# Kernel tuning notes

Measured on AMD Instinct MI355X. Metric: run time of the kernel, lower is better.

## Reference

```python
import jax, jax.numpy as jnp
import numpy as np

B, H, W, C = 8, 128, 128, 192
WS, SS, HEADS = 8, 4, 6
NW = (H // WS) * (W // WS)
N = WS * WS

def _rel_pos_index(ws):
    coords = np.stack(np.meshgrid(np.arange(ws), np.arange(ws), indexing='ij')).reshape(2, -1)
    rel = (coords[:, :, None] - coords[:, None, :]).transpose(1, 2, 0)
    rel[:, :, 0] += ws - 1
    rel[:, :, 1] += ws - 1
    rel[:, :, 0] *= 2 * ws - 1
    return rel.sum(-1)  # (N, N) int

REL_IDX = jnp.asarray(_rel_pos_index(WS).reshape(-1))

def setup_inputs():
    key = jax.random.key(0)
    ks = jax.random.split(key, 8)
    p = lambda k, shp: jax.random.normal(k, shp, jnp.float32) * 0.02
    # exact Swin shift mask for shift=(SS,SS)
    img = np.zeros((1, H, W, 1), np.float32)
    cnt = 0
    for hs in (slice(0, -WS), slice(-WS, -SS), slice(-SS, None)):
        for vs in (slice(0, -WS), slice(-WS, -SS), slice(-SS, None)):
            img[:, hs, vs, :] = cnt; cnt += 1
    mw = img.reshape(1, H // WS, WS, W // WS, WS, 1).transpose(0, 1, 3, 2, 4, 5).reshape(-1, N)
    diff = mw[:, None, :] - mw[:, :, None]
    mask = np.where(diff != 0, -100.0, 0.0).astype(np.float32)
    return dict(
        x=jax.random.normal(ks[0], (B, H, W, C), jnp.float32),
        mask_matrix=jnp.asarray(mask),
        norm1_g=jnp.ones((C,), jnp.float32), norm1_b=jnp.zeros((C,), jnp.float32),
        qkv_w=p(ks[1], (C, 3 * C)), qkv_b=jnp.zeros((3 * C,), jnp.float32),
        rel_bias_table=p(ks[2], ((2 * WS - 1) * (2 * WS - 1), HEADS)),
        proj_w=p(ks[3], (C, C)), proj_b=jnp.zeros((C,), jnp.float32),
        norm2_g=jnp.ones((C,), jnp.float32), norm2_b=jnp.zeros((C,), jnp.float32),
        fc1_w=p(ks[4], (C, 4 * C)), fc1_b=jnp.zeros((4 * C,), jnp.float32),
        fc2_w=p(ks[5], (4 * C, C)), fc2_b=jnp.zeros((C,), jnp.float32),
    )

def _ln(x, g, b):
    m = x.mean(-1, keepdims=True)
    v = x.var(-1, keepdims=True)
    return (x - m) * jax.lax.rsqrt(v + 1e-5) * g + b

def _window_attn(xw, mask, qkv_w, qkv_b, rel_bias_table, proj_w, proj_b):
    Bw = xw.shape[0]
    hd = C // HEADS
    scale = hd ** -0.5
    # ---- spatial window attention ----
    qkv = (xw @ qkv_w + qkv_b).reshape(Bw, N, 3, HEADS, hd).transpose(2, 0, 3, 1, 4)
    q, k, v = qkv[0], qkv[1], qkv[2]  # (Bw, heads, N, hd)
    attn = jnp.einsum('bhnd,bhmd->bhnm', q, k) * scale
    bias = rel_bias_table[REL_IDX].reshape(N, N, HEADS).transpose(2, 0, 1)
    attn = attn + bias[None]
    attn = attn.reshape(Bw // NW, NW, HEADS, N, N) + mask[None, :, None]
    attn = jax.nn.softmax(attn.reshape(Bw, HEADS, N, N), axis=-1)
    x_spatial = jnp.einsum('bhnm,bhmd->bhnd', attn, v).transpose(0, 2, 1, 3).reshape(Bw, N, C)
    # ---- Fourier-domain attention branch ----
    x2d = xw.reshape(Bw, WS, WS, C)
    xf = jnp.fft.rfftn(x2d, axes=(1, 2), norm='ortho')  # (Bw, WS, WS//2+1, C) complex
    Hf, Wf = xf.shape[1], xf.shape[2]
    Nf = Hf * Wf
    def _qkv(r):  # shared qkv linear applied to real/imag parts (bias in both)
        return (r.reshape(Bw, Nf, C) @ qkv_w + qkv_b).reshape(Bw, Nf, 3, HEADS, hd).transpose(2, 0, 3, 1, 4)
    qr, qi = _qkv(xf.real), _qkv(xf.imag)
    qf = jax.lax.complex(qr[0], qi[0])
    kf = jax.lax.complex(qr[1], qi[1])
    vf = jax.lax.complex(qr[2], qi[2])
    attn_f = jnp.einsum('bhnd,bhmd->bhnm', qf, kf) * scale  # plain transpose, no conj (matches torch)
    attn_mag = jax.nn.softmax(jnp.abs(attn_f), axis=-1)
    xf_res = jnp.einsum('bhnm,bhmd->bhnd', attn_mag.astype(jnp.complex64), vf)
    xf_res = xf_res.transpose(0, 2, 1, 3).reshape(Bw, Hf, Wf, C)
    x_four = jnp.fft.irfftn(xf_res, s=(WS, WS), axes=(1, 2), norm='ortho').reshape(Bw, N, C)
    return (x_spatial + x_four) @ proj_w + proj_b

def reference(x, mask_matrix, norm1_g, norm1_b, qkv_w, qkv_b, rel_bias_table,
              proj_w, proj_b, norm2_g, norm2_b, fc1_w, fc1_b, fc2_w, fc2_b):
    shortcut = x
    xn = _ln(x, norm1_g, norm1_b)
    # shift (H,W divisible by WS so no padding needed)
    xs = jnp.roll(xn, (-SS, -SS), axis=(1, 2))
    # window partition -> (B*nW, N, C)
    xw = xs.reshape(B, H // WS, WS, W // WS, WS, C).transpose(0, 1, 3, 2, 4, 5).reshape(-1, N, C)
    aw = _window_attn(xw, mask_matrix, qkv_w, qkv_b, rel_bias_table, proj_w, proj_b)
    # window reverse + unshift
    xs = aw.reshape(B, H // WS, W // WS, WS, WS, C).transpose(0, 1, 3, 2, 4, 5).reshape(B, H, W, C)
    xo = jnp.roll(xs, (SS, SS), axis=(1, 2))
    x1 = shortcut + xo
    y = _ln(x1, norm2_g, norm2_b)
    y = jax.nn.gelu(y @ fc1_w + fc1_b, approximate=False) @ fc2_w + fc2_b
    return x1 + y
```

## Files before the change

kernel.cpp:

```cpp
#include <hip/hip_runtime.h>
#include <hip/hip_bf16.h>
#include <math.h>

#define SSH 4
#define SCALE 0.17677669529663687f

typedef __bf16 bf16x8 __attribute__((ext_vector_type(8)));
typedef __bf16 bf16x4 __attribute__((ext_vector_type(4)));
typedef unsigned short ushort8 __attribute__((ext_vector_type(8)));
typedef float  f32x4  __attribute__((ext_vector_type(4)));

static __device__ __forceinline__ f32x4 mfma16(bf16x8 a, bf16x8 b, f32x4 c){
    return __builtin_amdgcn_mfma_f32_16x16x32_bf16(a, b, c, 0, 0, 0);
}
#define MFMA16(a,b,c) mfma16((a),(b),(c))

static __device__ __forceinline__ bf16x8 ldfrag(const __bf16* p){
    return *reinterpret_cast<const bf16x8*>(p);
}
static __device__ __forceinline__ f32x4 zero4(){
    f32x4 z; z[0]=0.f; z[1]=0.f; z[2]=0.f; z[3]=0.f; return z;
}
static __device__ __forceinline__ float gelu_fast(float x){
    float u = x*(0.7978845608f + 0.0356774081f*x*x);
    return __fdividef(x, 1.f + __expf(-2.f*u));
}

__global__ __launch_bounds__(256) void k_prep(const float* __restrict__ qkvw,
        const float* __restrict__ projw, const float* __restrict__ fc1w,
        const float* __restrict__ fc2w, __bf16* __restrict__ Wq,
        __bf16* __restrict__ Wp, __bf16* __restrict__ W1, __bf16* __restrict__ W2,
        __bf16* __restrict__ Fre, __bf16* __restrict__ Fim,
        __bf16* __restrict__ Ci,  __bf16* __restrict__ nSi){
    int i = blockIdx.x*256 + threadIdx.x;
    if (i < 110592){ int n = i/192, k = i - n*192; Wq[i] = (__bf16)qkvw[k*576 + n]; }
    if (i < 36864) { int n = i/192, k = i - n*192; Wp[i] = (__bf16)projw[k*192 + n]; }
    if (i < 147456){ int n = i/192, k = i - n*192; W1[i] = (__bf16)fc1w[k*768 + n]; }
    if (i < 147456){ int n = i/768, k = i - n*768; W2[i] = (__bf16)fc2w[k*192 + n]; }
    if (i < 3072){
        int n = i>>6, p = i&63;
        float vr = 0.f, vi = 0.f;
        if (n < 40){
            int u = n/5, v = n - u*5, r = p>>3, c = p&7;
            int k = (u*r + v*c)&7;
            float ang = (float)k * 0.78539816339744831f;
            vr = cosf(ang)*0.125f; vi = -sinf(ang)*0.125f;
        }
        Fre[i] = (__bf16)vr; Fim[i] = (__bf16)vi;
    }
    if (i < 4096){
        int p = i>>6, n = i&63;
        float vc = 0.f, vs = 0.f;
        if (n < 40){
            int u = n/5, v = n - u*5, r = p>>3, c = p&7;
            int k = (u*r + v*c)&7;
            float ang = (float)k * 0.78539816339744831f;
            float wv = (v>=1 && v<=3)? 2.f : 1.f;
            vc = wv*cosf(ang)*0.125f; vs = -wv*sinf(ang)*0.125f;
        }
        Ci[i] = (__bf16)vc; nSi[i] = (__bf16)vs;
    }
}

__global__ __launch_bounds__(256,2) void k_qkv(const float* __restrict__ x,
        const float* __restrict__ n1g, const float* __restrict__ n1b,
        const __bf16* __restrict__ Wqt, const float* __restrict__ qkv_b,
        __bf16* __restrict__ S){
    __shared__ __align__(16) __bf16 xw[64*200];
    __shared__ __align__(16) __bf16 Wt[192*72];
    __shared__ __align__(16) __bf16 Ss[64*200];
    int tid = threadIdx.x;
    int win = blockIdx.x;
    int bb = win>>8, rem = win&255, wh = rem>>4, wwi = rem&15;
    {
        int tok = tid>>2, part = tid&3;
        int r = tok>>3, c = tok&7;
        int sh = (wh*8 + r + SSH)&127, sw = (wwi*8 + c + SSH)&127;
        const float* srcp = x + (((size_t)(bb*128+sh))*128 + sw)*192 + part*48;
        float v[48];
        #pragma unroll
        for (int i=0;i<12;i++){
            float4 t4 = *reinterpret_cast<const float4*>(srcp + i*4);
            v[i*4]=t4.x; v[i*4+1]=t4.y; v[i*4+2]=t4.z; v[i*4+3]=t4.w;
        }
        float s=0.f, ss=0.f;
        #pragma unroll
        for (int i=0;i<48;i++){ s+=v[i]; ss+=v[i]*v[i]; }
        s  += __shfl_xor(s,1);  s  += __shfl_xor(s,2);
        ss += __shfl_xor(ss,1); ss += __shfl_xor(ss,2);
        float mean = s*(1.f/192.f);
        float rstd = rsqrtf(ss*(1.f/192.f) - mean*mean + 1e-5f);
        #pragma unroll
        for (int i8=0;i8<6;i8++){
            bf16x8 pk;
            #pragma unroll
            for (int j=0;j<8;j++){
                int ch = part*48 + i8*8 + j;
                pk[j] = (__bf16)((v[i8*8+j]-mean)*rstd*n1g[ch] + n1b[ch]);
            }
            *reinterpret_cast<bf16x8*>(&xw[tok*200 + part*48 + i8*8]) = pk;
        }
    }
    int lane = tid&63, w = tid>>6, lr = lane&15, lg = lane>>4;
    ushort8 wreg[6];
    auto ldW = [&](int s, ushort8* wr){
        int nc = s/3, kc = s - nc*3;
        #pragma unroll
        for (int i=0;i<6;i++){
            int e = tid + i*256;
            int j = e>>3, k8 = e&7;
            wr[i] = *reinterpret_cast<const ushort8*>(
                reinterpret_cast<const unsigned short*>(Wqt) + (size_t)(nc*192+j)*192 + kc*64 + k8*8);
        }
    };
    auto stW = [&](ushort8* wr){
        #pragma unroll
        for (int i=0;i<6;i++){
            int e = tid + i*256;
            int j = e>>3, k8 = e&7;
            *reinterpret_cast<ushort8*>(reinterpret_cast<unsigned short*>(Wt) + j*72 + k8*8) = wr[i];
        }
    };
    ldW(0, wreg);
    __syncthreads();
    stW(wreg);
    __syncthreads();
    f32x4 acc[4][3];
    #pragma unroll
    for (int m=0;m<4;m++)
        #pragma unroll
        for (int n=0;n<3;n++) acc[m][n] = zero4();
    for (int s=0; s<9; s++){
        int nc = s/3, kc = s - nc*3;
        if (s<8) ldW(s+1, wreg);
        #pragma unroll
        for (int kk=0; kk<2; kk++){
            int ko = kc*64 + kk*32 + lg*8;
            bf16x8 a[4];
            #pragma unroll
            for (int m=0;m<4;m++) a[m] = ldfrag(&xw[(16*m+lr)*200 + ko]);
            int klo = kk*32 + lg*8;
            bf16x8 bfr[3];
            #pragma unroll
            for (int n=0;n<3;n++) bfr[n] = ldfrag(&Wt[(48*w+16*n+lr)*72 + klo]);
            #pragma unroll
            for (int m=0;m<4;m++)
                #pragma unroll
                for (int n=0;n<3;n++) acc[m][n] = MFMA16(a[m], bfr[n], acc[m][n]);
        }
        if (kc==2){
            #pragma unroll
            for (int n=0;n<3;n++){
                int colL = 48*w + 16*n + lr;
                float bias = qkv_b[nc*192 + colL];
                #pragma unroll
                for (int m=0;m<4;m++)
                    #pragma unroll
                    for (int r=0;r<4;r++){
                        Ss[(16*m + 4*lg + r)*200 + colL] = (__bf16)(acc[m][n][r] + bias);
                        acc[m][n][r] = 0.f;
                    }
            }
        }
        __syncthreads();
        if (kc==2){
            #pragma unroll
            for (int i=0;i<6;i++){
                int e = tid + i*256;
                int row = e/24, c8 = e - row*24;
                *reinterpret_cast<bf16x8*>(S + (size_t)(win*64+row)*576 + nc*192 + c8*8) =
                    *reinterpret_cast<const bf16x8*>(&Ss[row*200 + c8*8]);
            }
        }
        if (s<8) stW(wreg);
        __syncthreads();
    }
}

__global__ __launch_bounds__(256,4) void k_spatial(const __bf16* __restrict__ S,
        const float* __restrict__ relt, const float* __restrict__ mask,
        float* __restrict__ Bbuf){
    __shared__ __align__(16) __bf16 P[64*72];
    __shared__ __align__(16) __bf16 Vt[32*72];
    __shared__ float reltL[1350];
    int tid = threadIdx.x;
    int win = blockIdx.x;
    int widx = win & 255;
    int lane = tid&63, w = tid>>6, lr = lane&15, lg = lane>>4;
    for (int e=tid; e<1350; e+=256) reltL[e] = relt[e];
    float mreg[16];
    int bidx[16];
    #pragma unroll
    for (int nt=0; nt<4; nt++)
        #pragma unroll
        for (int r=0;r<4;r++){
            int row = 16*w + 4*lg + r;
            int col = 16*nt + lr;
            mreg[nt*4+r] = mask[((widx*64 + row)<<6) + col];
            int dr = (row>>3)-(col>>3)+7, dc = (row&7)-(col&7)+7;
            bidx[nt*4+r] = (dr*15+dc)*6;
        }
    const size_t sbase = (size_t)win*64*576;
    const __bf16* Sq = S + sbase;
    const __bf16* Sk = S + sbase + 192;
    const __bf16* Sv = S + sbase + 384;
    for (int h=0; h<6; h++){
        __syncthreads();
        {
            int d = tid&31, pg = tid>>5;
            const __bf16* sp = Sv + (size_t)(pg*8)*576 + h*32 + d;
            bf16x4 v0, v1;
            v0[0]=sp[0];    v0[1]=sp[576];  v0[2]=sp[1152]; v0[3]=sp[1728];
            v1[0]=sp[2304]; v1[1]=sp[2880]; v1[2]=sp[3456]; v1[3]=sp[4032];
            *reinterpret_cast<bf16x4*>(&Vt[d*72 + pg*8])   = v0;
            *reinterpret_cast<bf16x4*>(&Vt[d*72 + pg*8+4]) = v1;
        }
        __syncthreads();
        bf16x8 aq = ldfrag(Sq + (size_t)(16*w+lr)*576 + h*32 + lg*8);
        f32x4 acc[4];
        #pragma unroll
        for (int nt=0;nt<4;nt++){
            bf16x8 bk = ldfrag(Sk + (size_t)(16*nt+lr)*576 + h*32 + lg*8);
            acc[nt] = MFMA16(aq, bk, zero4());
        }
        float p[16];
        #pragma unroll
        for (int r=0;r<4;r++){
            float sc[4];
            #pragma unroll
            for (int nt=0;nt<4;nt++)
                sc[nt] = acc[nt][r]*SCALE + reltL[bidx[nt*4+r] + h] + mreg[nt*4+r];
            float mx = fmaxf(fmaxf(sc[0],sc[1]),fmaxf(sc[2],sc[3]));
            mx = fmaxf(mx, __shfl_xor(mx,1));
            mx = fmaxf(mx, __shfl_xor(mx,2));
            mx = fmaxf(mx, __shfl_xor(mx,4));
            mx = fmaxf(mx, __shfl_xor(mx,8));
            float sum = 0.f;
            #pragma unroll
            for (int nt=0;nt<4;nt++){ sc[nt] = __expf(sc[nt]-mx); sum += sc[nt]; }
            sum += __shfl_xor(sum,1);
            sum += __shfl_xor(sum,2);
            sum += __shfl_xor(sum,4);
            sum += __shfl_xor(sum,8);
            float inv = 1.f/sum;
            #pragma unroll
            for (int nt=0;nt<4;nt++) p[r*4+nt] = sc[nt]*inv;
        }
        #pragma unroll
        for (int r=0;r<4;r++)
            #pragma unroll
            for (int nt=0;nt<4;nt++)
                P[(16*w + 4*lg + r)*72 + 16*nt + lr] = (__bf16)p[r*4+nt];
        #pragma unroll
        for (int dt=0; dt<2; dt++){
            f32x4 o = zero4();
            #pragma unroll
            for (int ks=0; ks<2; ks++)
                o = MFMA16(ldfrag(&P[(16*w+lr)*72 + ks*32 + lg*8]),
                           ldfrag(&Vt[(16*dt+lr)*72 + ks*32 + lg*8]), o);
            #pragma unroll
            for (int r=0;r<4;r++){
                int row = 16*w + 4*lg + r;
                Bbuf[((size_t)win*64 + row)*192 + h*32 + 16*dt + lr] = o[r];
            }
        }
    }
}

__global__ __launch_bounds__(256,3) void k_fattn(const __bf16* __restrict__ S,
        const float* __restrict__ qkv_b,
        const __bf16* __restrict__ Fre_g, const __bf16* __restrict__ Fim_g,
        const __bf16* __restrict__ Ci_g,  const __bf16* __restrict__ nSi_g,
        float* __restrict__ Bbuf){
    __shared__ __align__(16) unsigned char arena[51968];
    __bf16* Gq_r = (__bf16*)(arena);
    __bf16* Gqin = (__bf16*)(arena + 3840);
    __bf16* Gk_r = (__bf16*)(arena + 7680);
    __bf16* Gk_i = (__bf16*)(arena + 11520);
    __bf16* Rt_r = (__bf16*)(arena);
    __bf16* Rt_i = (__bf16*)(arena + 5632);
    __bf16* Gv_r = (__bf16*)(arena + 15360);
    __bf16* Gv_i = (__bf16*)(arena + 20992);
    __bf16* St3  = (__bf16*)(arena + 26624);
    float*  Smat = (float*) (arena + 26624);
    __bf16* P    = (__bf16*)(arena + 43520);
    int tid = threadIdx.x;
    int win = blockIdx.x / 6, h = blockIdx.x - win*6;
    int lane = tid&63, w = tid>>6, lr = lane&15, lg = lane>>4;
    bf16x4 z4; z4[0]=z4[1]=z4[2]=z4[3]=(__bf16)0.f;
    const size_t sbase = (size_t)win*64*576 + h*32;
    {
        int t2 = tid & 127;
        __bf16* A = (tid<128)? Gv_r : Gv_i;
        int row = t2>>2, c4 = (t2&3)*4;
        *reinterpret_cast<bf16x4*>(A + row*88 + 48 + c4) = z4;
    }
    {
        int d = tid&31, pg = tid>>5;
        #pragma unroll
        for (int m=0;m<3;m++){
            const __bf16* sp = S + sbase + (size_t)m*192 + (size_t)pg*8*576 + d;
            bf16x4 v0, v1;
            v0[0]=sp[0];      v0[1]=sp[576];    v0[2]=sp[1152];   v0[3]=sp[1728];
            v1[0]=sp[2304];   v1[1]=sp[2880];   v1[2]=sp[3456];   v1[3]=sp[4032];
            *reinterpret_cast<bf16x4*>(&St3[m*2816 + d*88 + pg*8])     = v0;
            *reinterpret_cast<bf16x4*>(&St3[m*2816 + d*88 + pg*8 + 4]) = v1;
        }
    }
    __syncthreads();
    for (int j=w; j<36; j+=4){
        int m = j/12, jj = j - m*12;
        int term = jj/6, r2 = jj - term*6;
        const __bf16* Stm = &St3[m*2816];
        if (m<2){
            int mt = r2>>1, nt = r2&1;
            const __bf16* Ag = (term? Fim_g : Fre_g) + (16*mt+lr)*64 + lg*8;
            f32x4 acc = zero4();
            acc = MFMA16(*reinterpret_cast<const bf16x8*>(Ag),
                         ldfrag(&Stm[(16*nt+lr)*88 + lg*8]), acc);
            acc = MFMA16(*reinterpret_cast<const bf16x8*>(Ag+32),
                         ldfrag(&Stm[(16*nt+lr)*88 + 32 + lg*8]), acc);
            int d = 16*nt + lr;
            float b = qkv_b[m*192 + h*32 + d];
            __bf16* dst = (m==0)? (term? Gqin : Gq_r) : (term? Gk_i : Gk_r);
            #pragma unroll
            for (int r=0;r<4;r++){
                int n = 16*mt + 4*lg + r;
                float val = acc[r] + ((term==0) ? ((n==0)? -7.f*b : b) : b);
                if (m==0 && term==1) val = -val;
                dst[n*40 + d] = (__bf16)val;
            }
        } else {
            int mt = r2/3, nt = r2 - mt*3;
            const __bf16* Bg = (term? Fim_g : Fre_g) + (16*nt+lr)*64 + lg*8;
            f32x4 acc = zero4();
            acc = MFMA16(ldfrag(&Stm[(16*mt+lr)*88 + lg*8]),
                         *reinterpret_cast<const bf16x8*>(Bg), acc);
            acc = MFMA16(ldfrag(&Stm[(16*mt+lr)*88 + 32 + lg*8]),
                         *reinterpret_cast<const bf16x8*>(Bg+32), acc);
            int n = 16*nt + lr;
            __bf16* dst = term? Gv_i : Gv_r;
            #pragma unroll
            for (int r=0;r<4;r++){
                int d = 16*mt + 4*lg + r;
                float b = qkv_b[2*192 + h*32 + d];
                float val = acc[r] + ((term==0) ? ((n==0)? -7.f*b : b) : b);
                dst[d*88 + n] = (__bf16)val;
            }
        }
    }
    __syncthreads();
    for (int j=w; j<9; j+=4){
        int mt = j/3, nt = j - mt*3;
        bf16x8 qr = ldfrag(&Gq_r[(16*mt+lr)*40 + lg*8]);
        bf16x8 qi = ldfrag(&Gqin[(16*mt+lr)*40 + lg*8]);
        bf16x8 kr = ldfrag(&Gk_r[(16*nt+lr)*40 + lg*8]);
        bf16x8 ki = ldfrag(&Gk_i[(16*nt+lr)*40 + lg*8]);
        f32x4 sre = MFMA16(qi, ki, zero4());
        sre = MFMA16(qr, kr, sre);
        f32x4 t1 = MFMA16(qr, ki, zero4());
        f32x4 t2 = MFMA16(qi, kr, zero4());
        #pragma unroll
        for (int r=0;r<4;r++){
            float sim = t1[r] - t2[r];
            Smat[(16*mt + 4*lg + r)*52 + 16*nt + lr] =
                SCALE * sqrtf(sre[r]*sre[r] + sim*sim);
        }
    }
    __syncthreads();
    if (tid < 160){
        int row = tid>>2, part = tid&3, e0 = part*10;
        float mx = -1e30f;
        #pragma unroll
        for (int j=0;j<10;j++) mx = fmaxf(mx, Smat[row*52 + e0 + j]);
        mx = fmaxf(mx, __shfl_xor(mx,1));
        mx = fmaxf(mx, __shfl_xor(mx,2));
        float ex[10]; float sum=0.f;
        #pragma unroll
        for (int j=0;j<10;j++){ ex[j] = __expf(Smat[row*52+e0+j]-mx); sum += ex[j]; }
        sum += __shfl_xor(sum,1);
        sum += __shfl_xor(sum,2);
        float inv = 1.f/sum;
        #pragma unroll
        for (int j=0;j<10;j++) Smat[row*52+e0+j] = ex[j]*inv;
    }
    __syncthreads();
    for (int e=tid; e<3072; e+=256){
        int row = e>>6, col = e&63;
        float v = (row<40 && col<40)? Smat[row*52+col] : 0.f;
        P[row*88+col] = (__bf16)v;
    }
    {
        int t2 = tid & 127;
        __bf16* A = (tid<128)? Rt_r : Rt_i;
        int row = t2>>2, c4 = (t2&3)*4;
        *reinterpret_cast<bf16x4*>(A + row*88 + 48 + c4) = z4;
    }
    __syncthreads();
    for (int j=w; j<12; j+=4){
        int term = j/6, r2 = j - term*6;
        int dt = r2/3, nt = r2 - dt*3;
        const __bf16* Gv = term? Gv_i : Gv_r;
        f32x4 acc = zero4();
        #pragma unroll
        for (int ks=0; ks<2; ks++)
            acc = MFMA16(ldfrag(&Gv[(16*dt+lr)*88 + ks*32 + lg*8]),
                         ldfrag(&P [(16*nt+lr)*88 + ks*32 + lg*8]), acc);
        __bf16* dst = term? Rt_i : Rt_r;
        #pragma unroll
        for (int r=0;r<4;r++)
            dst[(16*dt + 4*lg + r)*88 + 16*nt + lr] = (__bf16)acc[r];
    }
    __syncthreads();
    for (int j=w; j<8; j+=4){
        int dt = j>>2, pt = j&3;
        f32x4 acc = zero4();
        #pragma unroll
        for (int ks=0; ks<2; ks++)
            acc = MFMA16(*reinterpret_cast<const bf16x8*>(nSi_g + (16*pt+lr)*64 + ks*32 + lg*8),
                         ldfrag(&Rt_i[(16*dt+lr)*88 + ks*32 + lg*8]), acc);
        #pragma unroll
        for (int ks=0; ks<2; ks++)
            acc = MFMA16(*reinterpret_cast<const bf16x8*>(Ci_g + (16*pt+lr)*64 + ks*32 + lg*8),
                         ldfrag(&Rt_r[(16*dt+lr)*88 + ks*32 + lg*8]), acc);
        #pragma unroll
        for (int r=0;r<4;r++){
            int p = 16*pt + 4*lg + r, d = 16*dt + lr;
            size_t idx = ((size_t)win*64 + p)*192 + h*32 + d;
            Bbuf[idx] += acc[r];
        }
    }
}

__global__ __launch_bounds__(256,2) void k_ffn(const float* __restrict__ Bbuf,
        const float* __restrict__ x, const __bf16* __restrict__ Wpt,
        const float* __restrict__ proj_b, const float* __restrict__ g2,
        const float* __restrict__ b2v, const __bf16* __restrict__ W1t,
        const float* __restrict__ fc1b, const __bf16* __restrict__ W2t,
        const float* __restrict__ fc2b, float* __restrict__ out){
    __shared__ __align__(16) __bf16 xt[64*200];
    __shared__ __align__(16) __bf16 yb[64*200];
    int tid = threadIdx.x;
    int win = blockIdx.x;
    {
        int tok = tid>>2, part = tid&3;
        const float* srcp = Bbuf + ((size_t)win*64 + tok)*192 + part*48;
        #pragma unroll
        for (int i8=0;i8<6;i8++){
            float4 a4 = *reinterpret_cast<const float4*>(srcp + i8*8);
            float4 b4 = *reinterpret_cast<const float4*>(srcp + i8*8 + 4);
            bf16x8 pk;
            pk[0]=(__bf16)a4.x; pk[1]=(__bf16)a4.y; pk[2]=(__bf16)a4.z; pk[3]=(__bf16)a4.w;
            pk[4]=(__bf16)b4.x; pk[5]=(__bf16)b4.y; pk[6]=(__bf16)b4.z; pk[7]=(__bf16)b4.w;
            *reinterpret_cast<bf16x8*>(&xt[tok*200 + part*48 + i8*8]) = pk;
        }
    }
    __syncthreads();
    int lane = tid&63, w = tid>>6, lr = lane&15, lg = lane>>4;
    f32x4 acc[4][3];
    #pragma unroll
    for (int m=0;m<4;m++)
        #pragma unroll
        for (int n=0;n<3;n++) acc[m][n] = zero4();
    #pragma unroll
    for (int kc=0; kc<6; kc++){
        int ko = kc*32 + lg*8;
        bf16x8 a[4];
        #pragma unroll
        for (int m=0;m<4;m++) a[m] = ldfrag(&xt[(16*m+lr)*200 + ko]);
        bf16x8 bfr[3];
        #pragma unroll
        for (int n=0;n<3;n++)
            bfr[n] = ldfrag(Wpt + (size_t)(48*w + 16*n + lr)*192 + ko);
        #pragma unroll
        for (int m=0;m<4;m++)
            #pragma unroll
            for (int n=0;n<3;n++) acc[m][n] = MFMA16(a[m], bfr[n], acc[m][n]);
    }
    int bb = win>>8, rem = win&255, wh = rem>>4, wwi = rem&15;
    bf16x4 yreg[4][3];
    #pragma unroll
    for (int m=0;m<4;m++)
        #pragma unroll
        for (int r=0;r<4;r++){
            int t = 16*m + 4*lg + r;
            int p = wh*8 + (t>>3), q = wwi*8 + (t&7);
            int hh = (p+SSH)&127, w2 = (q+SSH)&127;
            size_t pixb = (((size_t)bb*128 + hh)*128 + w2)*192;
            #pragma unroll
            for (int n=0;n<3;n++){
                int col = 48*w + 16*n + lr;
                float yv = acc[m][n][r] + proj_b[col] + x[pixb + col];
                __bf16 yh = (__bf16)yv;
                yreg[m][n][r] = yh;
                yb[t*200 + col] = yh;
            }
        }
    __syncthreads();
    {
        int tok = tid>>2, part = tid&3;
        float v[48];
        #pragma unroll
        for (int i8=0;i8<6;i8++){
            bf16x8 pk = *reinterpret_cast<const bf16x8*>(&yb[tok*200 + part*48 + i8*8]);
            #pragma unroll
            for (int j=0;j<8;j++) v[i8*8+j] = (float)pk[j];
        }
        float s=0.f, ss=0.f;
        #pragma unroll
        for (int i=0;i<48;i++){ s+=v[i]; ss+=v[i]*v[i]; }
        s  += __shfl_xor(s,1);  s  += __shfl_xor(s,2);
        ss += __shfl_xor(ss,1); ss += __shfl_xor(ss,2);
        float mean = s*(1.f/192.f);
        float rstd = rsqrtf(ss*(1.f/192.f) - mean*mean + 1e-5f);
        #pragma unroll
        for (int i8=0;i8<6;i8++){
            bf16x8 pk;
            #pragma unroll
            for (int j=0;j<8;j++){
                int ch = part*48 + i8*8 + j;
                pk[j] = (__bf16)((v[i8*8+j]-mean)*rstd*g2[ch] + b2v[ch]);
            }
            *reinterpret_cast<bf16x8*>(&yb[tok*200 + part*48 + i8*8]) = pk;
        }
    }
    __syncthreads();
    f32x4 acc2[4][3];
    #pragma unroll
    for (int m=0;m<4;m++)
        #pragma unroll
        for (int n=0;n<3;n++) acc2[m][n] = zero4();
    for (int hc=0; hc<4; hc++){
        f32x4 acc1[4][3];
        #pragma unroll
        for (int m=0;m<4;m++)
            #pragma unroll
            for (int n=0;n<3;n++) acc1[m][n] = zero4();
        #pragma unroll
        for (int kc=0; kc<6; kc++){
            int ko = kc*32 + lg*8;
            bf16x8 a[4];
            #pragma unroll
            for (int m=0;m<4;m++) a[m] = ldfrag(&yb[(16*m+lr)*200 + ko]);
            bf16x8 bfr[3];
            #pragma unroll
            for (int n=0;n<3;n++)
                bfr[n] = ldfrag(W1t + (size_t)(hc*192 + 48*w + 16*n + lr)*192 + ko);
            #pragma unroll
            for (int m=0;m<4;m++)
                #pragma unroll
                for (int n=0;n<3;n++) acc1[m][n] = MFMA16(a[m], bfr[n], acc1[m][n]);
        }
        #pragma unroll
        for (int n=0;n<3;n++){
            int jcol = 48*w + 16*n + lr;
            float b1 = fc1b[hc*192 + jcol];
            #pragma unroll
            for (int m=0;m<4;m++)
                #pragma unroll
                for (int r=0;r<4;r++){
                    float xv = acc1[m][n][r] + b1;
                    xt[(16*m + 4*lg + r)*200 + jcol] = (__bf16)gelu_fast(xv);
                }
        }
        __syncthreads();
        #pragma unroll
        for (int kc=0; kc<6; kc++){
            int ko = kc*32 + lg*8;
            bf16x8 a[4];
            #pragma unroll
            for (int m=0;m<4;m++) a[m] = ldfrag(&xt[(16*m+lr)*200 + ko]);
            bf16x8 bfr[3];
            #pragma unroll
            for (int n=0;n<3;n++)
                bfr[n] = ldfrag(W2t + (size_t)(48*w + 16*n + lr)*768 + hc*192 + ko);
            #pragma unroll
            for (int m=0;m<4;m++)
                #pragma unroll
                for (int n=0;n<3;n++) acc2[m][n] = MFMA16(a[m], bfr[n], acc2[m][n]);
        }
        __syncthreads();
    }
    #pragma unroll
    for (int m=0;m<4;m++)
        #pragma unroll
        for (int r=0;r<4;r++){
            int t = 16*m + 4*lg + r;
            int p = wh*8 + (t>>3), q = wwi*8 + (t&7);
            int hh = (p+SSH)&127, w2 = (q+SSH)&127;
            size_t pixb = (((size_t)bb*128 + hh)*128 + w2)*192;
            #pragma unroll
            for (int n=0;n<3;n++){
                int col = 48*w + 16*n + lr;
                out[pixb + col] = acc2[m][n][r] + fc2b[col] + (float)yreg[m][n][r];
            }
        }
}

extern "C" void kernel_launch(void* const* d_in, const int* in_sizes, int n_in,
                              void* d_out, int out_size, void* d_ws, size_t ws_size,
                              hipStream_t stream) {
    const float* x     = (const float*)d_in[0];
    const float* mask  = (const float*)d_in[1];
    const float* n1g   = (const float*)d_in[2];
    const float* n1b   = (const float*)d_in[3];
    const float* qkvw  = (const float*)d_in[4];
    const float* qkvb  = (const float*)d_in[5];
    const float* relt  = (const float*)d_in[6];
    const float* projw = (const float*)d_in[7];
    const float* projb = (const float*)d_in[8];
    const float* n2g   = (const float*)d_in[9];
    const float* n2b   = (const float*)d_in[10];
    const float* fc1w  = (const float*)d_in[11];
    const float* fc1b  = (const float*)d_in[12];
    const float* fc2w  = (const float*)d_in[13];
    const float* fc2b  = (const float*)d_in[14];
    float* out = (float*)d_out;

    char* wsb = (char*)d_ws;
    __bf16* Sb   = (__bf16*)wsb;
    float*  Bbuf = (float*)(wsb + 150994944);
    __bf16* Wqt = (__bf16*)(wsb + 251658240);
    __bf16* Wpt = (__bf16*)(wsb + 251879424);
    __bf16* W1t = (__bf16*)(wsb + 251953152);
    __bf16* W2t = (__bf16*)(wsb + 252248064);
    __bf16* Fre = (__bf16*)(wsb + 252542976);
    __bf16* Fim = (__bf16*)(wsb + 252549120);
    __bf16* Ci  = (__bf16*)(wsb + 252555264);
    __bf16* nSi = (__bf16*)(wsb + 252563456);

    k_prep   <<<576,   256, 0, stream>>>(qkvw, projw, fc1w, fc2w, Wqt, Wpt, W1t, W2t,
                                         Fre, Fim, Ci, nSi);
    k_qkv    <<<2048,  256, 0, stream>>>(x, n1g, n1b, Wqt, qkvb, Sb);
    k_spatial<<<2048,  256, 0, stream>>>(Sb, relt, mask, Bbuf);
    k_fattn  <<<12288, 256, 0, stream>>>(Sb, qkvb, Fre, Fim, Ci, nSi, Bbuf);
    k_ffn    <<<2048,  256, 0, stream>>>(Bbuf, x, Wpt, projb, n2g, n2b,
                                         W1t, fc1b, W2t, fc2b, out);
}
```

Measured before the change: 595.4 us.

## Fuse spatial and Fourier window attention into one kernel with bf16 output

Merges the spatial attention kernel and the per-head Fourier attention kernel into a single per-window kernel. Both branches accumulate into a shared-memory bf16 tile that is written once to a bf16 buffer, and the FFN kernel reads that buffer directly as its MFMA A-operand. This removes the fp32 Bbuf write, its read-modify-write, the separate reread, and one launch. In exchange the Fourier parallelism drops from 12288 blocks to 2048, each looping over 6 heads, and occupancy falls because of the larger shared memory and launch_bounds(256,2). The spatial+Fourier sum is also rounded to bf16.

Result: slower. 620.1 us (+4.1%).

```diff
diff --git a/kernel.cpp b/kernel.cpp
--- a/kernel.cpp
+++ b/kernel.cpp
@@ -177,102 +177,17 @@
     }
 }
 
-__global__ __launch_bounds__(256,4) void k_spatial(const __bf16* __restrict__ S,
+__global__ __launch_bounds__(256,2) void k_attn(const __bf16* __restrict__ S,
         const float* __restrict__ relt, const float* __restrict__ mask,
-        float* __restrict__ Bbuf){
-    __shared__ __align__(16) __bf16 P[64*72];
-    __shared__ __align__(16) __bf16 Vt[32*72];
-    __shared__ float reltL[1350];
-    int tid = threadIdx.x;
-    int win = blockIdx.x;
-    int widx = win & 255;
-    int lane = tid&63, w = tid>>6, lr = lane&15, lg = lane>>4;
-    for (int e=tid; e<1350; e+=256) reltL[e] = relt[e];
-    float mreg[16];
-    int bidx[16];
-    #pragma unroll
-    for (int nt=0; nt<4; nt++)
-        #pragma unroll
-        for (int r=0;r<4;r++){
-            int row = 16*w + 4*lg + r;
-            int col = 16*nt + lr;
-            mreg[nt*4+r] = mask[((widx*64 + row)<<6) + col];
-            int dr = (row>>3)-(col>>3)+7, dc = (row&7)-(col&7)+7;
-            bidx[nt*4+r] = (dr*15+dc)*6;
-        }
-    const size_t sbase = (size_t)win*64*576;
-    const __bf16* Sq = S + sbase;
-    const __bf16* Sk = S + sbase + 192;
-    const __bf16* Sv = S + sbase + 384;
-    for (int h=0; h<6; h++){
-        __syncthreads();
-        {
-            int d = tid&31, pg = tid>>5;
-            const __bf16* sp = Sv + (size_t)(pg*8)*576 + h*32 + d;
-            bf16x4 v0, v1;
-            v0[0]=sp[0];    v0[1]=sp[576];  v0[2]=sp[1152]; v0[3]=sp[1728];
-            v1[0]=sp[2304]; v1[1]=sp[2880]; v1[2]=sp[3456]; v1[3]=sp[4032];
-            *reinterpret_cast<bf16x4*>(&Vt[d*72 + pg*8])   = v0;
-            *reinterpret_cast<bf16x4*>(&Vt[d*72 + pg*8+4]) = v1;
-        }
-        __syncthreads();
-        bf16x8 aq = ldfrag(Sq + (size_t)(16*w+lr)*576 + h*32 + lg*8);
-        f32x4 acc[4];
-        #pragma unroll
-        for (int nt=0;nt<4;nt++){
-            bf16x8 bk = ldfrag(Sk + (size_t)(16*nt+lr)*576 + h*32 + lg*8);
-            acc[nt] = MFMA16(aq, bk, zero4());
-        }
-        float p[16];
-        #pragma unroll
-        for (int r=0;r<4;r++){
-            float sc[4];
-            #pragma unroll
-            for (int nt=0;nt<4;nt++)
-                sc[nt] = acc[nt][r]*SCALE + reltL[bidx[nt*4+r] + h] + mreg[nt*4+r];
-            float mx = fmaxf(fmaxf(sc[0],sc[1]),fmaxf(sc[2],sc[3]));
-            mx = fmaxf(mx, __shfl_xor(mx,1));
-            mx = fmaxf(mx, __shfl_xor(mx,2));
-            mx = fmaxf(mx, __shfl_xor(mx,4));
-            mx = fmaxf(mx, __shfl_xor(mx,8));
-            float sum = 0.f;
-            #pragma unroll
-            for (int nt=0;nt<4;nt++){ sc[nt] = __expf(sc[nt]-mx); sum += sc[nt]; }
-            sum += __shfl_xor(sum,1);
-            sum += __shfl_xor(sum,2);
-            sum += __shfl_xor(sum,4);
-            sum += __shfl_xor(sum,8);
-            float inv = 1.f/sum;
-            #pragma unroll
-            for (int nt=0;nt<4;nt++) p[r*4+nt] = sc[nt]*inv;
-        }
-        #pragma unroll
-        for (int r=0;r<4;r++)
-            #pragma unroll
-            for (int nt=0;nt<4;nt++)
-                P[(16*w + 4*lg + r)*72 + 16*nt + lr] = (__bf16)p[r*4+nt];
-        #pragma unroll
-        for (int dt=0; dt<2; dt++){
-            f32x4 o = zero4();
-            #pragma unroll
-            for (int ks=0; ks<2; ks++)
-                o = MFMA16(ldfrag(&P[(16*w+lr)*72 + ks*32 + lg*8]),
-                           ldfrag(&Vt[(16*dt+lr)*72 + ks*32 + lg*8]), o);
-            #pragma unroll
-            for (int r=0;r<4;r++){
-                int row = 16*w + 4*lg + r;
-                Bbuf[((size_t)win*64 + row)*192 + h*32 + 16*dt + lr] = o[r];
-            }
-        }
-    }
-}
-
-__global__ __launch_bounds__(256,3) void k_fattn(const __bf16* __restrict__ S,
         const float* __restrict__ qkv_b,
         const __bf16* __restrict__ Fre_g, const __bf16* __restrict__ Fim_g,
         const __bf16* __restrict__ Ci_g,  const __bf16* __restrict__ nSi_g,
-        float* __restrict__ Bbuf){
+        __bf16* __restrict__ Bb){
+    __shared__ __align__(16) __bf16 Ot[64*200];
     __shared__ __align__(16) unsigned char arena[51968];
+    float*  reltL = (float*) arena;
+    __bf16* Ps    = (__bf16*)(arena + 5408);
+    __bf16* Vt    = (__bf16*)(arena + 14624);
     __bf16* Gq_r = (__bf16*)(arena);
     __bf16* Gqin = (__bf16*)(arena + 3840);
     __bf16* Gk_r = (__bf16*)(arena + 7680);
@@ -283,180 +198,257 @@
     __bf16* Gv_i = (__bf16*)(arena + 20992);
     __bf16* St3  = (__bf16*)(arena + 26624);
     float*  Smat = (float*) (arena + 26624);
-    __bf16* P    = (__bf16*)(arena + 43520);
+    __bf16* Pf   = (__bf16*)(arena + 43520);
     int tid = threadIdx.x;
-    int win = blockIdx.x / 6, h = blockIdx.x - win*6;
+    int win = blockIdx.x;
+    int widx = win & 255;
     int lane = tid&63, w = tid>>6, lr = lane&15, lg = lane>>4;
     bf16x4 z4; z4[0]=z4[1]=z4[2]=z4[3]=(__bf16)0.f;
-    const size_t sbase = (size_t)win*64*576 + h*32;
-    {
-        int t2 = tid & 127;
-        __bf16* A = (tid<128)? Gv_r : Gv_i;
-        int row = t2>>2, c4 = (t2&3)*4;
-        *reinterpret_cast<bf16x4*>(A + row*88 + 48 + c4) = z4;
-    }
-    {
-        int d = tid&31, pg = tid>>5;
-        #pragma unroll
-        for (int m=0;m<3;m++){
-            const __bf16* sp = S + sbase + (size_t)m*192 + (size_t)pg*8*576 + d;
+    for (int e=tid; e<1350; e+=256) reltL[e] = relt[e];
+    float mreg[16];
+    int bidx[16];
+    #pragma unroll
+    for (int nt=0; nt<4; nt++)
+        #pragma unroll
+        for (int r=0;r<4;r++){
+            int row = 16*w + 4*lg + r;
+            int col = 16*nt + lr;
+            mreg[nt*4+r] = mask[((widx*64 + row)<<6) + col];
+            int dr = (row>>3)-(col>>3)+7, dc = (row&7)-(col&7)+7;
+            bidx[nt*4+r] = (dr*15+dc)*6;
+        }
+    const size_t sbase = (size_t)win*64*576;
+    const __bf16* Sq = S + sbase;
+    const __bf16* Sk = S + sbase + 192;
+    const __bf16* Sv = S + sbase + 384;
+    for (int h=0; h<6; h++){
+        __syncthreads();
+        {
+            int d = tid&31, pg = tid>>5;
+            const __bf16* sp = Sv + (size_t)(pg*8)*576 + h*32 + d;
             bf16x4 v0, v1;
-            v0[0]=sp[0];      v0[1]=sp[576];    v0[2]=sp[1152];   v0[3]=sp[1728];
-            v1[0]=sp[2304];   v1[1]=sp[2880];   v1[2]=sp[3456];   v1[3]=sp[4032];
-            *reinterpret_cast<bf16x4*>(&St3[m*2816 + d*88 + pg*8])     = v0;
-            *reinterpret_cast<bf16x4*>(&St3[m*2816 + d*88 + pg*8 + 4]) = v1;
+            v0[0]=sp[0];    v0[1]=sp[576];  v0[2]=sp[1152]; v0[3]=sp[1728];
+            v1[0]=sp[2304]; v1[1]=sp[2880]; v1[2]=sp[3456]; v1[3]=sp[4032];
+            *reinterpret_cast<bf16x4*>(&Vt[d*72 + pg*8])   = v0;
+            *reinterpret_cast<bf16x4*>(&Vt[d*72 + pg*8+4]) = v1;
+        }
+        __syncthreads();
+        bf16x8 aq = ldfrag(Sq + (size_t)(16*w+lr)*576 + h*32 + lg*8);
+        f32x4 acc[4];
+        #pragma unroll
+        for (int nt=0;nt<4;nt++){
+            bf16x8 bk = ldfrag(Sk + (size_t)(16*nt+lr)*576 + h*32 + lg*8);
+            acc[nt] = MFMA16(aq, bk, zero4());
+        }
+        float p[16];
+        #pragma unroll
+        for (int r=0;r<4;r++){
+            float sc[4];
+            #pragma unroll
+            for (int nt=0;nt<4;nt++)
+                sc[nt] = acc[nt][r]*SCALE + reltL[bidx[nt*4+r] + h] + mreg[nt*4+r];
+            float mx = fmaxf(fmaxf(sc[0],sc[1]),fmaxf(sc[2],sc[3]));
+            mx = fmaxf(mx, __shfl_xor(mx,1));
+            mx = fmaxf(mx, __shfl_xor(mx,2));
+            mx = fmaxf(mx, __shfl_xor(mx,4));
+            mx = fmaxf(mx, __shfl_xor(mx,8));
+            float sum = 0.f;
+            #pragma unroll
+            for (int nt=0;nt<4;nt++){ sc[nt] = __expf(sc[nt]-mx); sum += sc[nt]; }
+            sum += __shfl_xor(sum,1);
+            sum += __shfl_xor(sum,2);
+            sum += __shfl_xor(sum,4);
+            sum += __shfl_xor(sum,8);
+            float inv = 1.f/sum;
+            #pragma unroll
+            for (int nt=0;nt<4;nt++) p[r*4+nt] = sc[nt]*inv;
+        }
+        #pragma unroll
+        for (int r=0;r<4;r++)
+            #pragma unroll
+            for (int nt=0;nt<4;nt++)
+                Ps[(16*w + 4*lg + r)*72 + 16*nt + lr] = (__bf16)p[r*4+nt];
+        #pragma unroll
+        for (int dt=0; dt<2; dt++){
+            f32x4 o = zero4();
+            #pragma unroll
+            for (int ks=0; ks<2; ks++)
+                o = MFMA16(ldfrag(&Ps[(16*w+lr)*72 + ks*32 + lg*8]),
+                           ldfrag(&Vt[(16*dt+lr)*72 + ks*32 + lg*8]), o);
+            #pragma unroll
+            for (int r=0;r<4;r++){
+                int row = 16*w + 4*lg + r;
+                Ot[row*200 + h*32 + 16*dt + lr] = (__bf16)o[r];
+            }
+        }
+    }
+    for (int h=0; h<6; h++){
+        __syncthreads();
+        const size_t hbase = sbase + h*32;
+        {
+            int t2 = tid & 127;
+            __bf16* A = (tid<128)? Gv_r : Gv_i;
+            int row = t2>>2, c4 = (t2&3)*4;
+            *reinterpret_cast<bf16x4*>(A + row*88 + 48 + c4) = z4;
+        }
+        {
+            int d = tid&31, pg = tid>>5;
+            #pragma unroll
+            for (int m=0;m<3;m++){
+                const __bf16* sp = S + hbase + (size_t)m*192 + (size_t)pg*8*576 + d;
+                bf16x4 v0, v1;
+                v0[0]=sp[0];      v0[1]=sp[576];    v0[2]=sp[1152];   v0[3]=sp[1728];
+                v1[0]=sp[2304];   v1[1]=sp[2880];   v1[2]=sp[3456];   v1[3]=sp[4032];
+                *reinterpret_cast<bf16x4*>(&St3[m*2816 + d*88 + pg*8])     = v0;
+                *reinterpret_cast<bf16x4*>(&St3[m*2816 + d*88 + pg*8 + 4]) = v1;
+            }
+        }
+        __syncthreads();
+        for (int j=w; j<36; j+=4){
+            int m = j/12, jj = j - m*12;
+            int term = jj/6, r2 = jj - term*6;
+            const __bf16* Stm = &St3[m*2816];
+            if (m<2){
+                int mt = r2>>1, nt = r2&1;
+                const __bf16* Ag = (term? Fim_g : Fre_g) + (16*mt+lr)*64 + lg*8;
+                f32x4 acc = zero4();
+                acc = MFMA16(*reinterpret_cast<const bf16x8*>(Ag),
+                             ldfrag(&Stm[(16*nt+lr)*88 + lg*8]), acc);
+                acc = MFMA16(*reinterpret_cast<const bf16x8*>(Ag+32),
+                             ldfrag(&Stm[(16*nt+lr)*88 + 32 + lg*8]), acc);
+                int d = 16*nt + lr;
+                float b = qkv_b[m*192 + h*32 + d];
+                __bf16* dst = (m==0)? (term? Gqin : Gq_r) : (term? Gk_i : Gk_r);
+                #pragma unroll
+                for (int r=0;r<4;r++){
+                    int n = 16*mt + 4*lg + r;
+                    float val = acc[r] + ((term==0) ? ((n==0)? -7.f*b : b) : b);
+                    if (m==0 && term==1) val = -val;
+                    dst[n*40 + d] = (__bf16)val;
+                }
+            } else {
+                int mt = r2/3, nt = r2 - mt*3;
+                const __bf16* Bg = (term? Fim_g : Fre_g) + (16*nt+lr)*64 + lg*8;
+                f32x4 acc = zero4();
+                acc = MFMA16(ldfrag(&Stm[(16*mt+lr)*88 + lg*8]),
+                             *reinterpret_cast<const bf16x8*>(Bg), acc);
+                acc = MFMA16(ldfrag(&Stm[(16*mt+lr)*88 + 32 + lg*8]),
+                             *reinterpret_cast<const bf16x8*>(Bg+32), acc);
+                int n = 16*nt + lr;
+                __bf16* dst = term? Gv_i : Gv_r;
+                #pragma unroll
+                for (int r=0;r<4;r++){
+                    int d = 16*mt + 4*lg + r;
+                    float b = qkv_b[2*192 + h*32 + d];
+                    float val = acc[r] + ((term==0) ? ((n==0)? -7.f*b : b) : b);
+                    dst[d*88 + n] = (__bf16)val;
+                }
+            }
+        }
+        __syncthreads();
+        for (int j=w; j<9; j+=4){
+            int mt = j/3, nt = j - mt*3;
+            bf16x8 qr = ldfrag(&Gq_r[(16*mt+lr)*40 + lg*8]);
+            bf16x8 qi = ldfrag(&Gqin[(16*mt+lr)*40 + lg*8]);
+            bf16x8 kr = ldfrag(&Gk_r[(16*nt+lr)*40 + lg*8]);
+            bf16x8 ki = ldfrag(&Gk_i[(16*nt+lr)*40 + lg*8]);
+            f32x4 sre = MFMA16(qi, ki, zero4());
+            sre = MFMA16(qr, kr, sre);
+            f32x4 t1 = MFMA16(qr, ki, zero4());
+            f32x4 t2 = MFMA16(qi, kr, zero4());
+            #pragma unroll
+            for (int r=0;r<4;r++){
+                float sim = t1[r] - t2[r];
+                Smat[(16*mt + 4*lg + r)*52 + 16*nt + lr] =
+                    SCALE * sqrtf(sre[r]*sre[r] + sim*sim);
+            }
+        }
+        __syncthreads();
+        if (tid < 160){
+            int row = tid>>2, part = tid&3, e0 = part*10;
+            float mx = -1e30f;
+            #pragma unroll
+            for (int j=0;j<10;j++) mx = fmaxf(mx, Smat[row*52 + e0 + j]);
+            mx = fmaxf(mx, __shfl_xor(mx,1));
+            mx = fmaxf(mx, __shfl_xor(mx,2));
+            float ex[10]; float sum=0.f;
+            #pragma unroll
+            for (int j=0;j<10;j++){ ex[j] = __expf(Smat[row*52+e0+j]-mx); sum += ex[j]; }
+            sum += __shfl_xor(sum,1);
+            sum += __shfl_xor(sum,2);
+            float inv = 1.f/sum;
+            #pragma unroll
+            for (int j=0;j<10;j++) Smat[row*52+e0+j] = ex[j]*inv;
+        }
+        __syncthreads();
+        for (int e=tid; e<3072; e+=256){
+            int row = e>>6, col = e&63;
+            float v = (row<40 && col<40)? Smat[row*52+col] : 0.f;
+            Pf[row*88+col] = (__bf16)v;
+        }
+        {
+            int t2 = tid & 127;
+            __bf16* A = (tid<128)? Rt_r : Rt_i;
+            int row = t2>>2, c4 = (t2&3)*4;
+            *reinterpret_cast<bf16x4*>(A + row*88 + 48 + c4) = z4;
+        }
+        __syncthreads();
+        for (int j=w; j<12; j+=4){
+            int term = j/6, r2 = j - term*6;
+            int dt = r2/3, nt = r2 - dt*3;
+            const __bf16* Gv = term? Gv_i : Gv_r;
+            f32x4 acc = zero4();
+            #pragma unroll
+            for (int ks=0; ks<2; ks++)
+                acc = MFMA16(ldfrag(&Gv[(16*dt+lr)*88 + ks*32 + lg*8]),
+                             ldfrag(&Pf[(16*nt+lr)*88 + ks*32 + lg*8]), acc);
+            __bf16* dst = term? Rt_i : Rt_r;
+            #pragma unroll
+            for (int r=0;r<4;r++)
+                dst[(16*dt + 4*lg + r)*88 + 16*nt + lr] = (__bf16)acc[r];
+        }
+        __syncthreads();
+        for (int j=w; j<8; j+=4){
+            int dt = j>>2, pt = j&3;
+            f32x4 acc = zero4();
+            #pragma unroll
+            for (int ks=0; ks<2; ks++)
+                acc = MFMA16(*reinterpret_cast<const bf16x8*>(nSi_g + (16*pt+lr)*64 + ks*32 + lg*8),
+                             ldfrag(&Rt_i[(16*dt+lr)*88 + ks*32 + lg*8]), acc);
+            #pragma unroll
+            for (int ks=0; ks<2; ks++)
+                acc = MFMA16(*reinterpret_cast<const bf16x8*>(Ci_g + (16*pt+lr)*64 + ks*32 + lg*8),
+                             ldfrag(&Rt_r[(16*dt+lr)*88 + ks*32 + lg*8]), acc);
+            #pragma unroll
+            for (int r=0;r<4;r++){
+                int p = 16*pt + 4*lg + r, d = 16*dt + lr;
+                int idx = p*200 + h*32 + d;
+                Ot[idx] = (__bf16)((float)Ot[idx] + acc[r]);
+            }
         }
     }
     __syncthreads();
-    for (int j=w; j<36; j+=4){
-        int m = j/12, jj = j - m*12;
-        int term = jj/6, r2 = jj - term*6;
-        const __bf16* Stm = &St3[m*2816];
-        if (m<2){
-            int mt = r2>>1, nt = r2&1;
-            const __bf16* Ag = (term? Fim_g : Fre_g) + (16*mt+lr)*64 + lg*8;
-            f32x4 acc = zero4();
-            acc = MFMA16(*reinterpret_cast<const bf16x8*>(Ag),
-                         ldfrag(&Stm[(16*nt+lr)*88 + lg*8]), acc);
-            acc = MFMA16(*reinterpret_cast<const bf16x8*>(Ag+32),
-                         ldfrag(&Stm[(16*nt+lr)*88 + 32 + lg*8]), acc);
-            int d = 16*nt + lr;
-            float b = qkv_b[m*192 + h*32 + d];
-            __bf16* dst = (m==0)? (term? Gqin : Gq_r) : (term? Gk_i : Gk_r);
-            #pragma unroll
-            for (int r=0;r<4;r++){
-                int n = 16*mt + 4*lg + r;
-                float val = acc[r] + ((term==0) ? ((n==0)? -7.f*b : b) : b);
-                if (m==0 && term==1) val = -val;
-                dst[n*40 + d] = (__bf16)val;
-            }
-        } else {
-            int mt = r2/3, nt = r2 - mt*3;
-            const __bf16* Bg = (term? Fim_g : Fre_g) + (16*nt+lr)*64 + lg*8;
-            f32x4 acc = zero4();
-            acc = MFMA16(ldfrag(&Stm[(16*mt+lr)*88 + lg*8]),
-                         *reinterpret_cast<const bf16x8*>(Bg), acc);
-            acc = MFMA16(ldfrag(&Stm[(16*mt+lr)*88 + 32 + lg*8]),
-                         *reinterpret_cast<const bf16x8*>(Bg+32), acc);
-            int n = 16*nt + lr;
-            __bf16* dst = term? Gv_i : Gv_r;
-            #pragma unroll
-            for (int r=0;r<4;r++){
-                int d = 16*mt + 4*lg + r;
-                float b = qkv_b[2*192 + h*32 + d];
-                float val = acc[r] + ((term==0) ? ((n==0)? -7.f*b : b) : b);
-                dst[d*88 + n] = (__bf16)val;
-            }
-        }
-    }
-    __syncthreads();
-    for (int j=w; j<9; j+=4){
-        int mt = j/3, nt = j - mt*3;
-        bf16x8 qr = ldfrag(&Gq_r[(16*mt+lr)*40 + lg*8]);
-        bf16x8 qi = ldfrag(&Gqin[(16*mt+lr)*40 + lg*8]);
-        bf16x8 kr = ldfrag(&Gk_r[(16*nt+lr)*40 + lg*8]);
-        bf16x8 ki = ldfrag(&Gk_i[(16*nt+lr)*40 + lg*8]);
-        f32x4 sre = MFMA16(qi, ki, zero4());
-        sre = MFMA16(qr, kr, sre);
-        f32x4 t1 = MFMA16(qr, ki, zero4());
-        f32x4 t2 = MFMA16(qi, kr, zero4());
-        #pragma unroll
-        for (int r=0;r<4;r++){
-            float sim = t1[r] - t2[r];
-            Smat[(16*mt + 4*lg + r)*52 + 16*nt + lr] =
-                SCALE * sqrtf(sre[r]*sre[r] + sim*sim);
-        }
-    }
-    __syncthreads();
-    if (tid < 160){
-        int row = tid>>2, part = tid&3, e0 = part*10;
-        float mx = -1e30f;
-        #pragma unroll
-        for (int j=0;j<10;j++) mx = fmaxf(mx, Smat[row*52 + e0 + j]);
-        mx = fmaxf(mx, __shfl_xor(mx,1));
-        mx = fmaxf(mx, __shfl_xor(mx,2));
-        float ex[10]; float sum=0.f;
-        #pragma unroll
-        for (int j=0;j<10;j++){ ex[j] = __expf(Smat[row*52+e0+j]-mx); sum += ex[j]; }
-        sum += __shfl_xor(sum,1);
-        sum += __shfl_xor(sum,2);
-        float inv = 1.f/sum;
-        #pragma unroll
-        for (int j=0;j<10;j++) Smat[row*52+e0+j] = ex[j]*inv;
-    }
-    __syncthreads();
-    for (int e=tid; e<3072; e+=256){
-        int row = e>>6, col = e&63;
-        float v = (row<40 && col<40)? Smat[row*52+col] : 0.f;
-        P[row*88+col] = (__bf16)v;
-    }
-    {
-        int t2 = tid & 127;
-        __bf16* A = (tid<128)? Rt_r : Rt_i;
-        int row = t2>>2, c4 = (t2&3)*4;
-        *reinterpret_cast<bf16x4*>(A + row*88 + 48 + c4) = z4;
-    }
-    __syncthreads();
-    for (int j=w; j<12; j+=4){
-        int term = j/6, r2 = j - term*6;
-        int dt = r2/3, nt = r2 - dt*3;
-        const __bf16* Gv = term? Gv_i : Gv_r;
-        f32x4 acc = zero4();
-        #pragma unroll
-        for (int ks=0; ks<2; ks++)
-            acc = MFMA16(ldfrag(&Gv[(16*dt+lr)*88 + ks*32 + lg*8]),
-                         ldfrag(&P [(16*nt+lr)*88 + ks*32 + lg*8]), acc);
-        __bf16* dst = term? Rt_i : Rt_r;
-        #pragma unroll
-        for (int r=0;r<4;r++)
-            dst[(16*dt + 4*lg + r)*88 + 16*nt + lr] = (__bf16)acc[r];
-    }
-    __syncthreads();
-    for (int j=w; j<8; j+=4){
-        int dt = j>>2, pt = j&3;
-        f32x4 acc = zero4();
-        #pragma unroll
-        for (int ks=0; ks<2; ks++)
-            acc = MFMA16(*reinterpret_cast<const bf16x8*>(nSi_g + (16*pt+lr)*64 + ks*32 + lg*8),
-                         ldfrag(&Rt_i[(16*dt+lr)*88 + ks*32 + lg*8]), acc);
-        #pragma unroll
-        for (int ks=0; ks<2; ks++)
-            acc = MFMA16(*reinterpret_cast<const bf16x8*>(Ci_g + (16*pt+lr)*64 + ks*32 + lg*8),
-                         ldfrag(&Rt_r[(16*dt+lr)*88 + ks*32 + lg*8]), acc);
-        #pragma unroll
-        for (int r=0;r<4;r++){
-            int p = 16*pt + 4*lg + r, d = 16*dt + lr;
-            size_t idx = ((size_t)win*64 + p)*192 + h*32 + d;
-            Bbuf[idx] += acc[r];
-        }
-    }
-}
-
-__global__ __launch_bounds__(256,2) void k_ffn(const float* __restrict__ Bbuf,
+    #pragma unroll
+    for (int i=0;i<6;i++){
+        int e = tid + i*256;
+        int row = e/24, c8 = e - row*24;
+        *reinterpret_cast<bf16x8*>(Bb + (size_t)(win*64+row)*192 + c8*8) =
+            *reinterpret_cast<const bf16x8*>(&Ot[row*200 + c8*8]);
+    }
+}
+
+__global__ __launch_bounds__(256,2) void k_ffn(const __bf16* __restrict__ Bb,
         const float* __restrict__ x, const __bf16* __restrict__ Wpt,
         const float* __restrict__ proj_b, const float* __restrict__ g2,
         const float* __restrict__ b2v, const __bf16* __restrict__ W1t,
         const float* __restrict__ fc1b, const __bf16* __restrict__ W2t,
         const float* __restrict__ fc2b, float* __restrict__ out){
-    __shared__ __align__(16) __bf16 xt[64*200];
+    __shared__ __align__(16) __bf16 hb[64*200];
     __shared__ __align__(16) __bf16 yb[64*200];
     int tid = threadIdx.x;
     int win = blockIdx.x;
-    {
-        int tok = tid>>2, part = tid&3;
-        const float* srcp = Bbuf + ((size_t)win*64 + tok)*192 + part*48;
-        #pragma unroll
-        for (int i8=0;i8<6;i8++){
-            float4 a4 = *reinterpret_cast<const float4*>(srcp + i8*8);
-            float4 b4 = *reinterpret_cast<const float4*>(srcp + i8*8 + 4);
-            bf16x8 pk;
-            pk[0]=(__bf16)a4.x; pk[1]=(__bf16)a4.y; pk[2]=(__bf16)a4.z; pk[3]=(__bf16)a4.w;
-            pk[4]=(__bf16)b4.x; pk[5]=(__bf16)b4.y; pk[6]=(__bf16)b4.z; pk[7]=(__bf16)b4.w;
-            *reinterpret_cast<bf16x8*>(&xt[tok*200 + part*48 + i8*8]) = pk;
-        }
-    }
-    __syncthreads();
     int lane = tid&63, w = tid>>6, lr = lane&15, lg = lane>>4;
+    const __bf16* Ab = Bb + (size_t)win*64*192;
     f32x4 acc[4][3];
     #pragma unroll
     for (int m=0;m<4;m++)
@@ -467,7 +459,7 @@
         int ko = kc*32 + lg*8;
         bf16x8 a[4];
         #pragma unroll
-        for (int m=0;m<4;m++) a[m] = ldfrag(&xt[(16*m+lr)*200 + ko]);
+        for (int m=0;m<4;m++) a[m] = ldfrag(Ab + (size_t)(16*m+lr)*192 + ko);
         bf16x8 bfr[3];
         #pragma unroll
         for (int n=0;n<3;n++)
@@ -560,7 +552,7 @@
                 #pragma unroll
                 for (int r=0;r<4;r++){
                     float xv = acc1[m][n][r] + b1;
-                    xt[(16*m + 4*lg + r)*200 + jcol] = (__bf16)gelu_fast(xv);
+                    hb[(16*m + 4*lg + r)*200 + jcol] = (__bf16)gelu_fast(xv);
                 }
         }
         __syncthreads();
@@ -569,7 +561,7 @@
             int ko = kc*32 + lg*8;
             bf16x8 a[4];
             #pragma unroll
-            for (int m=0;m<4;m++) a[m] = ldfrag(&xt[(16*m+lr)*200 + ko]);
+            for (int m=0;m<4;m++) a[m] = ldfrag(&hb[(16*m+lr)*200 + ko]);
             bf16x8 bfr[3];
             #pragma unroll
             for (int n=0;n<3;n++)
@@ -618,8 +610,8 @@
     float* out = (float*)d_out;
 
     char* wsb = (char*)d_ws;
-    __bf16* Sb   = (__bf16*)wsb;
-    float*  Bbuf = (float*)(wsb + 150994944);
+    __bf16* Sb  = (__bf16*)wsb;
+    __bf16* Bb  = (__bf16*)(wsb + 150994944);
     __bf16* Wqt = (__bf16*)(wsb + 251658240);
     __bf16* Wpt = (__bf16*)(wsb + 251879424);
     __bf16* W1t = (__bf16*)(wsb + 251953152);
@@ -629,11 +621,10 @@
     __bf16* Ci  = (__bf16*)(wsb + 252555264);
     __bf16* nSi = (__bf16*)(wsb + 252563456);
 
-    k_prep   <<<576,   256, 0, stream>>>(qkvw, projw, fc1w, fc2w, Wqt, Wpt, W1t, W2t,
-                                         Fre, Fim, Ci, nSi);
-    k_qkv    <<<2048,  256, 0, stream>>>(x, n1g, n1b, Wqt, qkvb, Sb);
-    k_spatial<<<2048,  256, 0, stream>>>(Sb, relt, mask, Bbuf);
-    k_fattn  <<<12288, 256, 0, stream>>>(Sb, qkvb, Fre, Fim, Ci, nSi, Bbuf);
-    k_ffn    <<<2048,  256, 0, stream>>>(Bbuf, x, Wpt, projb, n2g, n2b,
-                                         W1t, fc1b, W2t, fc2b, out);
-}
+    k_prep <<<576,  256, 0, stream>>>(qkvw, projw, fc1w, fc2w, Wqt, Wpt, W1t, W2t,
+                                      Fre, Fim, Ci, nSi);
+    k_qkv  <<<2048, 256, 0, stream>>>(x, n1g, n1b, Wqt, qkvb, Sb);
+    k_attn <<<2048, 256, 0, stream>>>(Sb, relt, mask, qkvb, Fre, Fim, Ci, nSi, Bb);
+    k_ffn  <<<2048, 256, 0, stream>>>(Bb, x, Wpt, projb, n2g, n2b,
+                                      W1t, fc1b, W2t, fc2b, out);
+}
```
